# Optimization experiments

Hardware: AMD Instinct MI355X
Metric: run time of the kernel (lower is better)

Reference implementation:

```python
import jax, jax.numpy as jnp
import numpy as np

B, S, IN, D, H, L, M = 8, 1024, 256, 512, 8, 2, 64
DK = D // H
FF = 4 * D
EPS = 1e-5


def setup_inputs() -> dict:
    key = jax.random.key(0)
    ks = jax.random.split(key, 16)
    w = lambda k, shape: jax.random.normal(k, shape, jnp.float32) * 0.02
    return {
        "inputs": jax.random.normal(ks[0], (B, S, IN), jnp.float32),
        "lengths": jax.random.randint(ks[1], (B,), S // 2, S + 1),
        "W_in": w(ks[2], (IN, D)), "b_in": jnp.zeros((D,), jnp.float32),
        # per-layer stacked params (leading axis L) for lax.scan
        "Wq": w(ks[3], (L, D, D)), "bq": jnp.zeros((L, D), jnp.float32),
        "Wk": w(ks[4], (L, D, D)), "bk": jnp.zeros((L, D), jnp.float32),
        "Wv": w(ks[5], (L, D, D)), "bv": jnp.zeros((L, D), jnp.float32),
        "Wo": w(ks[6], (L, D, D)), "bo": jnp.zeros((L, D), jnp.float32),
        "rel_bias": w(ks[7], (L, H, 2 * M - 1)),
        "W1": w(ks[8], (L, D, FF)), "b1": jnp.zeros((L, FF), jnp.float32),
        "W2": w(ks[9], (L, FF, D)), "b2": jnp.zeros((L, D), jnp.float32),
        "g1": jnp.ones((L, D), jnp.float32), "be1": jnp.zeros((L, D), jnp.float32),
        "g2": jnp.ones((L, D), jnp.float32), "be2": jnp.zeros((L, D), jnp.float32),
        "gf": jnp.ones((D,), jnp.float32), "bef": jnp.zeros((D,), jnp.float32),
    }


def _ln(x, g, b):
    m = jnp.mean(x, axis=-1, keepdims=True)
    v = jnp.mean(jnp.square(x - m), axis=-1, keepdims=True)
    return (x - m) * jax.lax.rsqrt(v + EPS) * g + b


def _sinusoid_pe(seq_len, d_model):
    pos = jnp.arange(seq_len, dtype=jnp.float32)[:, None]
    div = jnp.exp(jnp.arange(0, d_model, 2, dtype=jnp.float32) * (-np.log(10000.0) / d_model))
    pe = jnp.zeros((seq_len, d_model), jnp.float32)
    pe = pe.at[:, 0::2].set(jnp.sin(pos * div))
    pe = pe.at[:, 1::2].set(jnp.cos(pos * div))
    return pe


def _encoder(inputs, lengths, W_in, b_in, Wq, bq, Wk, bk, Wv, bv, Wo, bo,
             rel_bias, W1, b1, W2, b2, g1, be1, g2, be2, gf, bef):
    x = inputs @ W_in + b_in                      # (B,S,D)
    x = x + _sinusoid_pe(S, D)[None]
    pad = jnp.arange(S)[None, :] >= lengths[:, None]   # (B,S) True = padded key

    r = jnp.arange(S)
    rel_idx = jnp.clip(r[:, None] - r[None, :], -(M - 1), M - 1) + (M - 1)  # (S,S)
    scale = 1.0 / np.sqrt(DK)

    def layer(x, p):
        (wq, bq_, wk, bk_, wv, bv_, wo, bo_, rb, w1, b1_, w2, b2_, g1_, be1_, g2_, be2_) = p
        # --- self-attention sublayer (pre-norm) ---
        h = _ln(x, g1_, be1_)
        q = (h @ wq + bq_).reshape(B, S, H, DK).transpose(0, 2, 1, 3)  # (B,H,S,DK)
        k = (h @ wk + bk_).reshape(B, S, H, DK).transpose(0, 2, 1, 3)
        v = (h @ wv + bv_).reshape(B, S, H, DK).transpose(0, 2, 1, 3)
        scores = jnp.einsum('bhqd,bhkd->bhqk', q, k) * scale
        scores = scores + rb[:, rel_idx][None]            # (H,S,S) relative bias
        scores = jnp.where(pad[:, None, None, :], -jnp.inf, scores)
        attn = jax.nn.softmax(scores, axis=-1)
        o = jnp.einsum('bhqk,bhkd->bhqd', attn, v)
        o = o.transpose(0, 2, 1, 3).reshape(B, S, D) @ wo + bo_
        x = x + o
        # --- FFN sublayer (pre-norm) ---
        h = _ln(x, g2_, be2_)
        x = x + (jax.nn.relu(h @ w1 + b1_) @ w2 + b2_)
        return x, None

    stacked = (Wq, bq, Wk, bk, Wv, bv, Wo, bo, rel_bias, W1, b1, W2, b2, g1, be1, g2, be2)
    x, _ = jax.lax.scan(layer, x, stacked)
    return _ln(x, gf, bef)


def reference(inputs, lengths, W_in, b_in, Wq, bq, Wk, bk, Wv, bv, Wo, bo,
              rel_bias, W1, b1, W2, b2, g1, be1, g2, be2, gf, bef):
    return _encoder(inputs, lengths, W_in, b_in, Wq, bq, Wk, bk, Wv, bv, Wo, bo,
                    rel_bias, W1, b1, W2, b2, g1, be1, g2, be2, gf, bef)
```

## Files before the change

kernel.cpp:

```cpp
#include <hip/hip_runtime.h>
#include <hip/hip_bf16.h>

typedef unsigned short u16;
typedef unsigned int u32;
typedef __bf16 v8bf __attribute__((ext_vector_type(8)));
typedef float v4f __attribute__((ext_vector_type(4)));

#define B_SZ 8
#define S_LEN 1024
#define IN_DIM 256
#define DMODEL 512
#define NHEAD 8
#define DK 64
#define FF_DIM 2048
#define MROWS (B_SZ * S_LEN)
#define QSCALE 0.1803368801111204f

__device__ __forceinline__ u16 f2bf(float f) {
    unsigned int x = __float_as_uint(f);
    unsigned int r = (x + 0x7fffu + ((x >> 16) & 1u)) >> 16;
    return (u16)r;
}

__device__ __forceinline__ void gl16(const u16* g, u16* l) {
    __builtin_amdgcn_global_load_lds((const __attribute__((address_space(1))) unsigned int*)g,
                                     (__attribute__((address_space(3))) unsigned int*)l, 16, 0, 0);
}

__global__ __launch_bounds__(256) void conv_bf16_kernel(const float* __restrict__ in,
                                                        u16* __restrict__ out, int n4) {
    int i = blockIdx.x * 256 + threadIdx.x;
    if (i < n4) {
        float4 v = ((const float4*)in)[i];
        ushort4 o;
        o.x = f2bf(v.x); o.y = f2bf(v.y); o.z = f2bf(v.z); o.w = f2bf(v.w);
        ((ushort4*)out)[i] = o;
    }
}

struct TDesc { const float* src; u16* dst; int K; int N; };
struct TArgs { TDesc d[13]; };

__global__ void transpose_conv_kernel(TArgs args) {
    TDesc t = args.d[blockIdx.z];
    int k0 = blockIdx.x * 32, n0 = blockIdx.y * 32;
    if (k0 >= t.K || n0 >= t.N) return;
    __shared__ float tile[32][33];
    int tx = threadIdx.x, ty = threadIdx.y;
#pragma unroll
    for (int j = 0; j < 4; j++) {
        int k = k0 + ty + j * 8;
        tile[ty + j * 8][tx] = t.src[(size_t)k * t.N + n0 + tx];
    }
    __syncthreads();
#pragma unroll
    for (int j = 0; j < 4; j++) {
        int n = n0 + ty + j * 8;
        t.dst[(size_t)n * t.K + k0 + tx] = f2bf(tile[tx][ty + j * 8]);
    }
}

template <bool OUT_BF16>
__global__ __launch_bounds__(256) void ln_kernel(const float* __restrict__ x,
                                                 const float* __restrict__ g,
                                                 const float* __restrict__ b,
                                                 void* __restrict__ out) {
    int row = blockIdx.x * 4 + (threadIdx.x >> 6);
    int lane = threadIdx.x & 63;
    const float4* xr = (const float4*)(x + (size_t)row * DMODEL);
    float4 v0 = xr[lane], v1 = xr[lane + 64];
    float s = v0.x + v0.y + v0.z + v0.w + v1.x + v1.y + v1.z + v1.w;
    float sq = v0.x * v0.x + v0.y * v0.y + v0.z * v0.z + v0.w * v0.w +
               v1.x * v1.x + v1.y * v1.y + v1.z * v1.z + v1.w * v1.w;
#pragma unroll
    for (int m = 1; m < 64; m <<= 1) {
        s += __shfl_xor(s, m);
        sq += __shfl_xor(sq, m);
    }
    float mean = s * (1.0f / DMODEL);
    float var = sq * (1.0f / DMODEL) - mean * mean;
    float rstd = rsqrtf(var + 1e-5f);
    const float4* g4 = (const float4*)g;
    const float4* b4 = (const float4*)b;
    float4 ga = g4[lane], gb = g4[lane + 64], ba = b4[lane], bb = b4[lane + 64];
    float4 r0, r1;
    r0.x = (v0.x - mean) * rstd * ga.x + ba.x;
    r0.y = (v0.y - mean) * rstd * ga.y + ba.y;
    r0.z = (v0.z - mean) * rstd * ga.z + ba.z;
    r0.w = (v0.w - mean) * rstd * ga.w + ba.w;
    r1.x = (v1.x - mean) * rstd * gb.x + bb.x;
    r1.y = (v1.y - mean) * rstd * gb.y + bb.y;
    r1.z = (v1.z - mean) * rstd * gb.z + bb.z;
    r1.w = (v1.w - mean) * rstd * gb.w + bb.w;
    if (OUT_BF16) {
        ushort4 o0, o1;
        o0.x = f2bf(r0.x); o0.y = f2bf(r0.y); o0.z = f2bf(r0.z); o0.w = f2bf(r0.w);
        o1.x = f2bf(r1.x); o1.y = f2bf(r1.y); o1.z = f2bf(r1.z); o1.w = f2bf(r1.w);
        ((ushort4*)out)[(size_t)row * 128 + lane] = o0;
        ((ushort4*)out)[(size_t)row * 128 + 64 + lane] = o1;
    } else {
        ((float4*)out)[(size_t)row * 128 + lane] = r0;
        ((float4*)out)[(size_t)row * 128 + 64 + lane] = r1;
    }
}

template <int MT, int NT>
__device__ __forceinline__ void gemm_core(const u16* __restrict__ A, const u16* __restrict__ Bt,
                                          int K, v4f (&acc)[MT][NT]) {
    constexpr int BM = MT * 32;
    constexpr int BN = NT * 32;
    __shared__ u16 As[BM * 64];
    __shared__ u16 Bs[BN * 64];
    int tid = threadIdx.x;
    int n0 = blockIdx.x * BN, m0 = blockIdx.y * BM;
    int w = tid >> 6, lane = tid & 63;
    int wr = (w >> 1) * (BM / 2), wc = (w & 1) * (BN / 2);
    int lr = lane & 15, lq = lane >> 4;
    int r8 = lane >> 3, cb = lane & 7;
    int scol = (cb ^ r8) * 8;

    v4f zero = {0.f, 0.f, 0.f, 0.f};
#pragma unroll
    for (int i = 0; i < MT; i++)
#pragma unroll
        for (int j = 0; j < NT; j++) acc[i][j] = zero;

    const u16* gA[MT]; u16* lA[MT];
#pragma unroll
    for (int j = 0; j < MT; j++) {
        int row0 = (MT * 8) * w + j * 8;
        gA[j] = A + (size_t)(m0 + row0 + r8) * K + scol;
        lA[j] = As + row0 * 64;
    }
    const u16* gB[NT]; u16* lB[NT];
#pragma unroll
    for (int j = 0; j < NT; j++) {
        int row0 = (NT * 8) * w + j * 8;
        gB[j] = Bt + (size_t)(n0 + row0 + r8) * K + scol;
        lB[j] = Bs + row0 * 64;
    }

    for (int k0 = 0; k0 < K; k0 += 64) {
#pragma unroll
        for (int j = 0; j < MT; j++) gl16(gA[j], lA[j]);
#pragma unroll
        for (int j = 0; j < NT; j++) gl16(gB[j], lB[j]);
        __syncthreads();
#pragma unroll
        for (int kk = 0; kk < 2; kk++) {
            int xb = ((kk * 4 + lq) ^ (lr & 7)) * 8;
            v8bf af[MT], bfr[NT];
#pragma unroll
            for (int i = 0; i < MT; i++)
                af[i] = *(const v8bf*)&As[(wr + i * 16 + lr) * 64 + xb];
#pragma unroll
            for (int j = 0; j < NT; j++)
                bfr[j] = *(const v8bf*)&Bs[(wc + j * 16 + lr) * 64 + xb];
#pragma unroll
            for (int mt = 0; mt < MT; mt++)
#pragma unroll
                for (int nt = 0; nt < NT; nt++)
                    acc[mt][nt] = __builtin_amdgcn_mfma_f32_16x16x32_bf16(af[mt], bfr[nt], acc[mt][nt], 0, 0, 0);
        }
        __syncthreads();
#pragma unroll
        for (int j = 0; j < MT; j++) gA[j] += 64;
#pragma unroll
        for (int j = 0; j < NT; j++) gB[j] += 64;
    }
}

__global__ __launch_bounds__(256) void gemm_in_kernel(const u16* __restrict__ A,
                                                      const u16* __restrict__ Bt,
                                                      const float* __restrict__ bias,
                                                      float* __restrict__ Out, int K) {
    v4f acc[4][2];
    gemm_core<4, 2>(A, Bt, K, acc);
    int tid = threadIdx.x, w = tid >> 6, lane = tid & 63;
    int lr = lane & 15, lq = lane >> 4;
    int wr = (w >> 1) * 64, wc = (w & 1) * 32;
    int n0 = blockIdx.x * 64, m0 = blockIdx.y * 128;
#pragma unroll
    for (int mt = 0; mt < 4; mt++) {
#pragma unroll
        for (int nt = 0; nt < 2; nt++) {
            int col = n0 + wc + nt * 16 + lr;
            float bcol = bias[col];
            float freq = __builtin_amdgcn_exp2f((float)(col & ~1) * (-0.025953277f));
#pragma unroll
            for (int reg = 0; reg < 4; reg++) {
                int row = m0 + wr + mt * 16 + lq * 4 + reg;
                float rev = (float)(row & (S_LEN - 1)) * freq * 0.15915494309189535f;
                float fr = __builtin_amdgcn_fractf(rev);
                float pe = (col & 1) ? __builtin_amdgcn_cosf(fr) : __builtin_amdgcn_sinf(fr);
                Out[(size_t)row * DMODEL + col] = acc[mt][nt][reg] + bcol + pe;
            }
        }
    }
}

__global__ __launch_bounds__(256) void gemm_qkv_kernel(const u16* __restrict__ A,
                                                       const u16* __restrict__ Bt,
                                                       const float* __restrict__ bq,
                                                       const float* __restrict__ bk,
                                                       const float* __restrict__ bv,
                                                       u16* __restrict__ Qo,
                                                       u16* __restrict__ Ko,
                                                       u16* __restrict__ Vto, int K) {
    v4f acc[4][4];
    gemm_core<4, 4>(A, Bt, K, acc);
    int tid = threadIdx.x, w = tid >> 6, lane = tid & 63;
    int lr = lane & 15, lq = lane >> 4;
    int wr = (w >> 1) * 64, wc = (w & 1) * 64;
    int n0 = blockIdx.x * 128, m0 = blockIdx.y * 128;
    int seg = n0 >> 9;
#pragma unroll
    for (int mt = 0; mt < 4; mt++) {
#pragma unroll
        for (int nt = 0; nt < 4; nt++) {
            int col = (n0 + wc + nt * 16 + lr) & (DMODEL - 1);
            if (seg == 0) {
                float bcol = bq[col];
#pragma unroll
                for (int reg = 0; reg < 4; reg++) {
                    int row = m0 + wr + mt * 16 + lq * 4 + reg;
                    Qo[(size_t)row * DMODEL + col] = f2bf((acc[mt][nt][reg] + bcol) * QSCALE);
                }
            } else if (seg == 1) {
                float bcol = bk[col];
#pragma unroll
                for (int reg = 0; reg < 4; reg++) {
                    int row = m0 + wr + mt * 16 + lq * 4 + reg;
                    Ko[(size_t)row * DMODEL + col] = f2bf(acc[mt][nt][reg] + bcol);
                }
            } else {
                float bcol = bv[col];
                int row0 = m0 + wr + mt * 16 + lq * 4;
                int bb = row0 >> 10, s0 = row0 & (S_LEN - 1);
                ushort4 o;
                o.x = f2bf(acc[mt][nt][0] + bcol);
                o.y = f2bf(acc[mt][nt][1] + bcol);
                o.z = f2bf(acc[mt][nt][2] + bcol);
                o.w = f2bf(acc[mt][nt][3] + bcol);
                *(ushort4*)(Vto + ((size_t)(bb * DMODEL + col)) * S_LEN + s0) = o;
            }
        }
    }
}

__global__ __launch_bounds__(256) void gemm_relu_kernel(const u16* __restrict__ A,
                                                        const u16* __restrict__ Bt,
                                                        const float* __restrict__ bias,
                                                        u16* __restrict__ Out, int N, int K) {
    v4f acc[4][4];
    gemm_core<4, 4>(A, Bt, K, acc);
    int tid = threadIdx.x, w = tid >> 6, lane = tid & 63;
    int lr = lane & 15, lq = lane >> 4;
    int wr = (w >> 1) * 64, wc = (w & 1) * 64;
    int n0 = blockIdx.x * 128, m0 = blockIdx.y * 128;
#pragma unroll
    for (int mt = 0; mt < 4; mt++) {
#pragma unroll
        for (int nt = 0; nt < 4; nt++) {
            int col = n0 + wc + nt * 16 + lr;
            float bcol = bias[col];
#pragma unroll
            for (int reg = 0; reg < 4; reg++) {
                int row = m0 + wr + mt * 16 + lq * 4 + reg;
                Out[(size_t)row * N + col] = f2bf(fmaxf(acc[mt][nt][reg] + bcol, 0.0f));
            }
        }
    }
}

__global__ __launch_bounds__(256) void gemm_res_kernel(const u16* __restrict__ A,
                                                       const u16* __restrict__ Bt,
                                                       const float* __restrict__ bias,
                                                       float* __restrict__ Out, int K) {
    v4f acc[4][2];
    gemm_core<4, 2>(A, Bt, K, acc);
    int tid = threadIdx.x, w = tid >> 6, lane = tid & 63;
    int lr = lane & 15, lq = lane >> 4;
    int wr = (w >> 1) * 64, wc = (w & 1) * 32;
    int n0 = blockIdx.x * 64, m0 = blockIdx.y * 128;
#pragma unroll
    for (int mt = 0; mt < 4; mt++) {
#pragma unroll
        for (int nt = 0; nt < 2; nt++) {
            int col = n0 + wc + nt * 16 + lr;
            float bcol = bias[col];
#pragma unroll
            for (int reg = 0; reg < 4; reg++) {
                int row = m0 + wr + mt * 16 + lq * 4 + reg;
                size_t idx = (size_t)row * DMODEL + col;
                Out[idx] = Out[idx] + acc[mt][nt][reg] + bcol;
            }
        }
    }
}

#define LDP 68
__global__ __launch_bounds__(256) void fattn_kernel(const u16* __restrict__ Qg,
                                                    const u16* __restrict__ Kg,
                                                    const u16* __restrict__ Vtg,
                                                    const float* __restrict__ rb,
                                                    const int* __restrict__ lengths,
                                                    u16* __restrict__ Op,
                                                    float* __restrict__ lsums) {
    int bid = blockIdx.x;
    int wg = (bid & 7) * 128 + (bid >> 3);
    int half = wg & 1;
    int qt = (wg >> 1) & 7;
    int bh = wg >> 4;
    int h = bh & 7, b = bh >> 3;
    int tid = threadIdx.x, w = tid >> 6, lane = tid & 63;
    int lr = lane & 15, lq = lane >> 4;
    __shared__ u16 Ks[2][64 * 64];
    __shared__ u16 Vs[2][64 * 64];
    __shared__ u16 Pw[4][32 * LDP];
    __shared__ float rbs[128];
    int len = lengths[b];
    if (tid < 127) rbs[tid] = rb[h * 127 + tid] * 1.4426950408889634f;

    int kstart = half * 512;
    int kend = half ? len : 512;

    int qw = qt * 128 + w * 32;
    v8bf qa[2][2];
#pragma unroll
    for (int ntq = 0; ntq < 2; ntq++) {
        size_t qrow = ((size_t)(b * S_LEN + qw + ntq * 16 + lr)) * DMODEL + h * DK;
        qa[ntq][0] = *(const v8bf*)(Qg + qrow + lq * 8);
        qa[ntq][1] = *(const v8bf*)(Qg + qrow + 32 + lq * 8);
    }

    v4f zero = {0.f, 0.f, 0.f, 0.f};
    v4f Oacc[2][4];
#pragma unroll
    for (int mt = 0; mt < 2; mt++)
#pragma unroll
        for (int nt = 0; nt < 4; nt++) Oacc[mt][nt] = zero;
    float lsum[2] = {0.f, 0.f};

    const u16* Kbase = Kg + ((size_t)b * S_LEN) * DMODEL + h * DK;
    const u16* Vbase = Vtg + ((size_t)(b * DMODEL + h * DK)) * S_LEN;
    u16* P = Pw[w];
    int r8 = lane >> 3, cb = lane & 7;
    int swz = (cb ^ r8) * 8;

#pragma unroll
    for (int j = 0; j < 2; j++) {
        int row0 = w * 16 + j * 8;
        gl16(Kbase + (size_t)(kstart + row0 + r8) * DMODEL + swz, Ks[0] + row0 * 64);
        gl16(Vbase + (size_t)(row0 + r8) * S_LEN + kstart + swz, Vs[0] + row0 * 64);
    }

    int pb = 0;
    for (int kb0 = kstart; kb0 < kend; kb0 += 64, pb ^= 1) {
        __syncthreads();
        __builtin_amdgcn_sched_barrier(0);

        int nxt = kb0 + 64;
        if (nxt < kend) {
#pragma unroll
            for (int j = 0; j < 2; j++) {
                int row0 = w * 16 + j * 8;
                gl16(Kbase + (size_t)(nxt + row0 + r8) * DMODEL + swz, Ks[pb ^ 1] + row0 * 64);
                gl16(Vbase + (size_t)(row0 + r8) * S_LEN + nxt + swz, Vs[pb ^ 1] + row0 * 64);
            }
        }
        const u16* Ksc = Ks[pb];
        const u16* Vsc = Vs[pb];

        v8bf kf[4][2];
#pragma unroll
        for (int mtk = 0; mtk < 4; mtk++) {
#pragma unroll
            for (int half_ = 0; half_ < 2; half_++) {
                int xb = ((half_ * 4 + lq) ^ (lr & 7)) * 8;
                kf[mtk][half_] = *(const v8bf*)&Ksc[(mtk * 16 + lr) * 64 + xb];
            }
        }

        v4f S[4][2];
        __builtin_amdgcn_s_setprio(1);
#pragma unroll
        for (int mtk = 0; mtk < 4; mtk++)
#pragma unroll
            for (int ntq = 0; ntq < 2; ntq++) {
                v4f s = __builtin_amdgcn_mfma_f32_16x16x32_bf16(kf[mtk][0], qa[ntq][0], zero, 0, 0, 0);
                S[mtk][ntq] = __builtin_amdgcn_mfma_f32_16x16x32_bf16(kf[mtk][1], qa[ntq][1], s, 0, 0, 0);
            }
        __builtin_amdgcn_s_setprio(0);

        bool edge = (kb0 + 64 > len);
        int dmin = qw - (kb0 + 63), dmax = qw + 31 - kb0;
        bool perel = !(dmax <= -63 || dmin >= 63);
        float bconst = (dmax <= -63) ? rbs[0] : rbs[126];
#pragma unroll
        for (int mtk = 0; mtk < 4; mtk++) {
#pragma unroll
            for (int ntq = 0; ntq < 2; ntq++) {
                int q = qw + ntq * 16 + lr;
                float p[4];
#pragma unroll
                for (int r = 0; r < 4; r++) {
                    int key = kb0 + mtk * 16 + lq * 4 + r;
                    float s = S[mtk][ntq][r];
                    if (perel) {
                        int d = q - key;
                        d = d < -63 ? -63 : (d > 63 ? 63 : d);
                        s += rbs[d + 63];
                    } else {
                        s += bconst;
                    }
                    float pv = __builtin_amdgcn_exp2f(s);
                    if (edge && key >= len) pv = 0.f;
                    lsum[ntq] += pv;
                    p[r] = pv;
                }
                uint2 pk;
                pk.x = (__float_as_uint(p[1]) & 0xffff0000u) | (__float_as_uint(p[0]) >> 16);
                pk.y = (__float_as_uint(p[3]) & 0xffff0000u) | (__float_as_uint(p[2]) >> 16);
                *(uint2*)&P[(ntq * 16 + lr) * LDP + mtk * 16 + lq * 4] = pk;
            }
        }

        v8bf vb[4][2];
#pragma unroll
        for (int ntd = 0; ntd < 4; ntd++) {
#pragma unroll
            for (int half_ = 0; half_ < 2; half_++) {
                int xb = ((half_ * 4 + lq) ^ (lr & 7)) * 8;
                vb[ntd][half_] = *(const v8bf*)&Vsc[(ntd * 16 + lr) * 64 + xb];
            }
        }
        __builtin_amdgcn_s_setprio(1);
#pragma unroll
        for (int mtq = 0; mtq < 2; mtq++) {
            v8bf pa0 = *(const v8bf*)&P[(mtq * 16 + lr) * LDP + lq * 8];
            v8bf pa1 = *(const v8bf*)&P[(mtq * 16 + lr) * LDP + 32 + lq * 8];
#pragma unroll
            for (int ntd = 0; ntd < 4; ntd++) {
                Oacc[mtq][ntd] = __builtin_amdgcn_mfma_f32_16x16x32_bf16(pa0, vb[ntd][0], Oacc[mtq][ntd], 0, 0, 0);
                Oacc[mtq][ntd] = __builtin_amdgcn_mfma_f32_16x16x32_bf16(pa1, vb[ntd][1], Oacc[mtq][ntd], 0, 0, 0);
            }
        }
        __builtin_amdgcn_s_setprio(0);
    }

    float lsumR[2];
#pragma unroll
    for (int ntq = 0; ntq < 2; ntq++) {
        float s = lsum[ntq];
        s += __shfl_xor(s, 16);
        s += __shfl_xor(s, 32);
        lsumR[ntq] = s;
    }
    if (lq == 0) {
#pragma unroll
        for (int ntq = 0; ntq < 2; ntq++) {
            int q = qw + ntq * 16 + lr;
            lsums[((size_t)half * MROWS + b * S_LEN + q) * NHEAD + h] = lsumR[ntq];
        }
    }
    u16* Oh = Op + (size_t)half * MROWS * DMODEL;
#pragma unroll
    for (int mtq = 0; mtq < 2; mtq++) {
        size_t obase = ((size_t)(b * S_LEN + qw + mtq * 16)) * DMODEL + h * DK;
#pragma unroll
        for (int ntd = 0; ntd < 4; ntd++)
#pragma unroll
            for (int r = 0; r < 4; r++)
                Oh[obase + (size_t)(lq * 4 + r) * DMODEL + ntd * 16 + lr] = f2bf(Oacc[mtq][ntd][r]);
    }
}

__device__ __forceinline__ u32 comb2(u32 a, u32 b, float inv) {
    float r0 = (__uint_as_float(a << 16) + __uint_as_float(b << 16)) * inv;
    float r1 = (__uint_as_float(a & 0xffff0000u) + __uint_as_float(b & 0xffff0000u)) * inv;
    return (u32)f2bf(r0) | ((u32)f2bf(r1) << 16);
}

__global__ __launch_bounds__(256) void attn_combine_kernel(const u16* __restrict__ Op,
                                                           const float* __restrict__ lsums,
                                                           u16* __restrict__ out) {
    int row = blockIdx.x * 4 + (threadIdx.x >> 6);
    int lane = threadIdx.x & 63;
    int h = lane >> 3;
    float l0 = lsums[(size_t)row * NHEAD + h];
    float l1 = lsums[((size_t)MROWS + row) * NHEAD + h];
    float inv = 1.0f / (l0 + l1);
    size_t base = (size_t)row * DMODEL + lane * 8;
    uint4 a = *(const uint4*)(Op + base);
    uint4 c = *(const uint4*)(Op + (size_t)MROWS * DMODEL + base);
    uint4 o;
    o.x = comb2(a.x, c.x, inv);
    o.y = comb2(a.y, c.y, inv);
    o.z = comb2(a.z, c.z, inv);
    o.w = comb2(a.w, c.w, inv);
    *(uint4*)(out + base) = o;
}

extern "C" void kernel_launch(void* const* d_in, const int* in_sizes, int n_in,
                              void* d_out, int out_size, void* d_ws, size_t ws_size,
                              hipStream_t stream) {
    const float* inputs   = (const float*)d_in[0];
    const int*   lengths  = (const int*)d_in[1];
    const float* W_in     = (const float*)d_in[2];
    const float* b_in     = (const float*)d_in[3];
    const float* Wq       = (const float*)d_in[4];
    const float* bq       = (const float*)d_in[5];
    const float* Wk       = (const float*)d_in[6];
    const float* bk       = (const float*)d_in[7];
    const float* Wv       = (const float*)d_in[8];
    const float* bv       = (const float*)d_in[9];
    const float* Wo       = (const float*)d_in[10];
    const float* bo       = (const float*)d_in[11];
    const float* rel_bias = (const float*)d_in[12];
    const float* W1       = (const float*)d_in[13];
    const float* b1       = (const float*)d_in[14];
    const float* W2       = (const float*)d_in[15];
    const float* b2       = (const float*)d_in[16];
    const float* g1       = (const float*)d_in[17];
    const float* be1      = (const float*)d_in[18];
    const float* g2       = (const float*)d_in[19];
    const float* be2      = (const float*)d_in[20];
    const float* gf       = (const float*)d_in[21];
    const float* bef      = (const float*)d_in[22];

    char* ws = (char*)d_ws;
    float* xbuf = (float*)ws;          ws += (size_t)MROWS * DMODEL * 4;
    u16* hbuf   = (u16*)ws;            ws += (size_t)MROWS * DMODEL * 2;
    u16* aobuf  = hbuf;
    u16* qbf    = (u16*)ws;            ws += (size_t)MROWS * FF_DIM * 2;
    u16* kbf    = qbf + (size_t)MROWS * DMODEL;
    u16* vtbf   = kbf + (size_t)MROWS * DMODEL;
    float* lsums = (float*)(vtbf + (size_t)MROWS * DMODEL);
    u16* tbuf   = qbf;
    u16* inbf   = qbf;
    u16* opart  = (u16*)d_out;
    u16* wt_in  = (u16*)ws;            ws += (size_t)DMODEL * IN_DIM * 2;
    u16 *qkvw[2], *wto[2], *wt1[2], *wt2[2];
    for (int l = 0; l < 2; l++) { qkvw[l] = (u16*)ws; ws += (size_t)3 * DMODEL * DMODEL * 2; }
    for (int l = 0; l < 2; l++) { wto[l] = (u16*)ws; ws += (size_t)DMODEL * DMODEL * 2; }
    for (int l = 0; l < 2; l++) { wt1[l] = (u16*)ws; ws += (size_t)FF_DIM * DMODEL * 2; }
    for (int l = 0; l < 2; l++) { wt2[l] = (u16*)ws; ws += (size_t)DMODEL * FF_DIM * 2; }

    TArgs ta;
    int ti = 0;
    ta.d[ti++] = {W_in, wt_in, IN_DIM, DMODEL};
    for (int l = 0; l < 2; l++) {
        ta.d[ti++] = {Wq + (size_t)l * DMODEL * DMODEL, qkvw[l], DMODEL, DMODEL};
        ta.d[ti++] = {Wk + (size_t)l * DMODEL * DMODEL, qkvw[l] + (size_t)DMODEL * DMODEL, DMODEL, DMODEL};
        ta.d[ti++] = {Wv + (size_t)l * DMODEL * DMODEL, qkvw[l] + (size_t)2 * DMODEL * DMODEL, DMODEL, DMODEL};
        ta.d[ti++] = {Wo + (size_t)l * DMODEL * DMODEL, wto[l], DMODEL, DMODEL};
        ta.d[ti++] = {W1 + (size_t)l * DMODEL * FF_DIM, wt1[l], DMODEL, FF_DIM};
        ta.d[ti++] = {W2 + (size_t)l * FF_DIM * DMODEL, wt2[l], FF_DIM, DMODEL};
    }

    conv_bf16_kernel<<<dim3((MROWS * IN_DIM / 4 + 255) / 256), 256, 0, stream>>>(
        inputs, inbf, MROWS * IN_DIM / 4);
    transpose_conv_kernel<<<dim3(64, 64, 13), dim3(32, 8), 0, stream>>>(ta);

    gemm_in_kernel<<<dim3(DMODEL / 64, MROWS / 128), 256, 0, stream>>>(
        inbf, wt_in, b_in, xbuf, IN_DIM);

    for (int l = 0; l < 2; l++) {
        ln_kernel<true><<<MROWS / 4, 256, 0, stream>>>(xbuf, g1 + l * DMODEL, be1 + l * DMODEL, hbuf);
        gemm_qkv_kernel<<<dim3(3 * DMODEL / 128, MROWS / 128), 256, 0, stream>>>(
            hbuf, qkvw[l], bq + l * DMODEL, bk + l * DMODEL, bv + l * DMODEL,
            qbf, kbf, vtbf, DMODEL);
        fattn_kernel<<<dim3(1024), 256, 0, stream>>>(
            qbf, kbf, vtbf, rel_bias + (size_t)l * NHEAD * 127, lengths, opart, lsums);
        attn_combine_kernel<<<MROWS / 4, 256, 0, stream>>>(opart, lsums, aobuf);
        gemm_res_kernel<<<dim3(DMODEL / 64, MROWS / 128), 256, 0, stream>>>(
            aobuf, wto[l], bo + l * DMODEL, xbuf, DMODEL);
        ln_kernel<true><<<MROWS / 4, 256, 0, stream>>>(xbuf, g2 + l * DMODEL, be2 + l * DMODEL, hbuf);
        gemm_relu_kernel<<<dim3(FF_DIM / 128, MROWS / 128), 256, 0, stream>>>(
            hbuf, wt1[l], b1 + l * FF_DIM, tbuf, FF_DIM, DMODEL);
        gemm_res_kernel<<<dim3(DMODEL / 64, MROWS / 128), 256, 0, stream>>>(
            tbuf, wt2[l], b2 + l * DMODEL, xbuf, FF_DIM);
    }
    ln_kernel<false><<<MROWS / 4, 256, 0, stream>>>(xbuf, gf, bef, d_out);
}
```

Measured before the change: 495.7 us.

## Keep attention probabilities in registers and balance key split by sequence length

The flash-attention kernel no longer stages P through shared memory. The exp'd scores stay in registers and feed the PV MFMA directly, with V read from LDS as the A operand and the output accumulator transposed to match. The key range is now split at half the padded length instead of a fixed 512, so both halves do similar work. The block-to-work mapping changes, launch bounds request 4 waves per SIMD, and output stores become 8-byte vector writes. The transposed V fragment gather uses narrower 8-byte LDS reads, and the occupancy hint may force register spills.

```diff
diff --git a/kernel.cpp b/kernel.cpp
--- a/kernel.cpp
+++ b/kernel.cpp
@@ -299,31 +299,31 @@
     }
 }
 
-#define LDP 68
-__global__ __launch_bounds__(256) void fattn_kernel(const u16* __restrict__ Qg,
-                                                    const u16* __restrict__ Kg,
-                                                    const u16* __restrict__ Vtg,
-                                                    const float* __restrict__ rb,
-                                                    const int* __restrict__ lengths,
-                                                    u16* __restrict__ Op,
-                                                    float* __restrict__ lsums) {
+__global__ __launch_bounds__(256, 4) void fattn_kernel(const u16* __restrict__ Qg,
+                                                       const u16* __restrict__ Kg,
+                                                       const u16* __restrict__ Vtg,
+                                                       const float* __restrict__ rb,
+                                                       const int* __restrict__ lengths,
+                                                       u16* __restrict__ Op,
+                                                       float* __restrict__ lsums) {
     int bid = blockIdx.x;
     int wg = (bid & 7) * 128 + (bid >> 3);
-    int half = wg & 1;
-    int qt = (wg >> 1) & 7;
-    int bh = wg >> 4;
-    int h = bh & 7, b = bh >> 3;
+    int i = wg & 127;
+    int h = wg >> 7;
+    int b = i & 7;
+    int qt = (i >> 3) & 7;
+    int kvh = (i >> 6) & 1;
     int tid = threadIdx.x, w = tid >> 6, lane = tid & 63;
     int lr = lane & 15, lq = lane >> 4;
     __shared__ u16 Ks[2][64 * 64];
     __shared__ u16 Vs[2][64 * 64];
-    __shared__ u16 Pw[4][32 * LDP];
     __shared__ float rbs[128];
     int len = lengths[b];
     if (tid < 127) rbs[tid] = rb[h * 127 + tid] * 1.4426950408889634f;
 
-    int kstart = half * 512;
-    int kend = half ? len : 512;
+    int l2 = ((len + 127) >> 7) << 6;
+    int kstart = kvh ? l2 : 0;
+    int kend = kvh ? len : l2;
 
     int qw = qt * 128 + w * 32;
     v8bf qa[2][2];
@@ -335,16 +335,15 @@
     }
 
     v4f zero = {0.f, 0.f, 0.f, 0.f};
-    v4f Oacc[2][4];
-#pragma unroll
-    for (int mt = 0; mt < 2; mt++)
-#pragma unroll
-        for (int nt = 0; nt < 4; nt++) Oacc[mt][nt] = zero;
+    v4f Oacc[4][2];
+#pragma unroll
+    for (int dt = 0; dt < 4; dt++)
+#pragma unroll
+        for (int nt = 0; nt < 2; nt++) Oacc[dt][nt] = zero;
     float lsum[2] = {0.f, 0.f};
 
     const u16* Kbase = Kg + ((size_t)b * S_LEN) * DMODEL + h * DK;
     const u16* Vbase = Vtg + ((size_t)(b * DMODEL + h * DK)) * S_LEN;
-    u16* P = Pw[w];
     int r8 = lane >> 3, cb = lane & 7;
     int swz = (cb ^ r8) * 8;
 
@@ -372,31 +371,27 @@
         const u16* Ksc = Ks[pb];
         const u16* Vsc = Vs[pb];
 
-        v8bf kf[4][2];
-#pragma unroll
-        for (int mtk = 0; mtk < 4; mtk++) {
-#pragma unroll
-            for (int half_ = 0; half_ < 2; half_++) {
-                int xb = ((half_ * 4 + lq) ^ (lr & 7)) * 8;
-                kf[mtk][half_] = *(const v8bf*)&Ksc[(mtk * 16 + lr) * 64 + xb];
-            }
-        }
-
         v4f S[4][2];
         __builtin_amdgcn_s_setprio(1);
 #pragma unroll
-        for (int mtk = 0; mtk < 4; mtk++)
+        for (int mtk = 0; mtk < 4; mtk++) {
+            int xb0 = (lq ^ (lr & 7)) * 8;
+            int xb1 = ((4 + lq) ^ (lr & 7)) * 8;
+            v8bf kf0 = *(const v8bf*)&Ksc[(mtk * 16 + lr) * 64 + xb0];
+            v8bf kf1 = *(const v8bf*)&Ksc[(mtk * 16 + lr) * 64 + xb1];
 #pragma unroll
             for (int ntq = 0; ntq < 2; ntq++) {
-                v4f s = __builtin_amdgcn_mfma_f32_16x16x32_bf16(kf[mtk][0], qa[ntq][0], zero, 0, 0, 0);
-                S[mtk][ntq] = __builtin_amdgcn_mfma_f32_16x16x32_bf16(kf[mtk][1], qa[ntq][1], s, 0, 0, 0);
-            }
+                v4f s = __builtin_amdgcn_mfma_f32_16x16x32_bf16(kf0, qa[ntq][0], zero, 0, 0, 0);
+                S[mtk][ntq] = __builtin_amdgcn_mfma_f32_16x16x32_bf16(kf1, qa[ntq][1], s, 0, 0, 0);
+            }
+        }
         __builtin_amdgcn_s_setprio(0);
 
         bool edge = (kb0 + 64 > len);
         int dmin = qw - (kb0 + 63), dmax = qw + 31 - kb0;
         bool perel = !(dmax <= -63 || dmin >= 63);
         float bconst = (dmax <= -63) ? rbs[0] : rbs[126];
+        uint2 pks[4][2];
 #pragma unroll
         for (int mtk = 0; mtk < 4; mtk++) {
 #pragma unroll
@@ -419,31 +414,29 @@
                     lsum[ntq] += pv;
                     p[r] = pv;
                 }
-                uint2 pk;
-                pk.x = (__float_as_uint(p[1]) & 0xffff0000u) | (__float_as_uint(p[0]) >> 16);
-                pk.y = (__float_as_uint(p[3]) & 0xffff0000u) | (__float_as_uint(p[2]) >> 16);
-                *(uint2*)&P[(ntq * 16 + lr) * LDP + mtk * 16 + lq * 4] = pk;
-            }
-        }
-
-        v8bf vb[4][2];
-#pragma unroll
-        for (int ntd = 0; ntd < 4; ntd++) {
-#pragma unroll
-            for (int half_ = 0; half_ < 2; half_++) {
-                int xb = ((half_ * 4 + lq) ^ (lr & 7)) * 8;
-                vb[ntd][half_] = *(const v8bf*)&Vsc[(ntd * 16 + lr) * 64 + xb];
-            }
-        }
+                pks[mtk][ntq].x = (__float_as_uint(p[1]) & 0xffff0000u) | (__float_as_uint(p[0]) >> 16);
+                pks[mtk][ntq].y = (__float_as_uint(p[3]) & 0xffff0000u) | (__float_as_uint(p[2]) >> 16);
+            }
+        }
+
         __builtin_amdgcn_s_setprio(1);
 #pragma unroll
-        for (int mtq = 0; mtq < 2; mtq++) {
-            v8bf pa0 = *(const v8bf*)&P[(mtq * 16 + lr) * LDP + lq * 8];
-            v8bf pa1 = *(const v8bf*)&P[(mtq * 16 + lr) * LDP + 32 + lq * 8];
-#pragma unroll
-            for (int ntd = 0; ntd < 4; ntd++) {
-                Oacc[mtq][ntd] = __builtin_amdgcn_mfma_f32_16x16x32_bf16(pa0, vb[ntd][0], Oacc[mtq][ntd], 0, 0, 0);
-                Oacc[mtq][ntd] = __builtin_amdgcn_mfma_f32_16x16x32_bf16(pa1, vb[ntd][1], Oacc[mtq][ntd], 0, 0, 0);
+        for (int kh = 0; kh < 2; kh++) {
+            uint4 tp0 = {pks[kh * 2][0].x, pks[kh * 2][0].y, pks[kh * 2 + 1][0].x, pks[kh * 2 + 1][0].y};
+            uint4 tp1 = {pks[kh * 2][1].x, pks[kh * 2][1].y, pks[kh * 2 + 1][1].x, pks[kh * 2 + 1][1].y};
+            v8bf pb0 = *(v8bf*)&tp0;
+            v8bf pb1 = *(v8bf*)&tp1;
+            int gl = kh * 4 + (lq >> 1);
+            int sub = (lq & 1) * 4;
+#pragma unroll
+            for (int dt = 0; dt < 4; dt++) {
+                int drow = (dt * 16 + lr) * 64;
+                uint2 lo = *(const uint2*)&Vsc[drow + ((gl ^ (lr & 7)) * 8 + sub)];
+                uint2 hi = *(const uint2*)&Vsc[drow + (((gl + 2) ^ (lr & 7)) * 8 + sub)];
+                uint4 tv = {lo.x, lo.y, hi.x, hi.y};
+                v8bf va = *(v8bf*)&tv;
+                Oacc[dt][0] = __builtin_amdgcn_mfma_f32_16x16x32_bf16(va, pb0, Oacc[dt][0], 0, 0, 0);
+                Oacc[dt][1] = __builtin_amdgcn_mfma_f32_16x16x32_bf16(va, pb1, Oacc[dt][1], 0, 0, 0);
             }
         }
         __builtin_amdgcn_s_setprio(0);
@@ -461,18 +454,22 @@
 #pragma unroll
         for (int ntq = 0; ntq < 2; ntq++) {
             int q = qw + ntq * 16 + lr;
-            lsums[((size_t)half * MROWS + b * S_LEN + q) * NHEAD + h] = lsumR[ntq];
-        }
-    }
-    u16* Oh = Op + (size_t)half * MROWS * DMODEL;
-#pragma unroll
-    for (int mtq = 0; mtq < 2; mtq++) {
-        size_t obase = ((size_t)(b * S_LEN + qw + mtq * 16)) * DMODEL + h * DK;
-#pragma unroll
-        for (int ntd = 0; ntd < 4; ntd++)
-#pragma unroll
-            for (int r = 0; r < 4; r++)
-                Oh[obase + (size_t)(lq * 4 + r) * DMODEL + ntd * 16 + lr] = f2bf(Oacc[mtq][ntd][r]);
+            lsums[((size_t)kvh * MROWS + b * S_LEN + q) * NHEAD + h] = lsumR[ntq];
+        }
+    }
+    u16* Oh = Op + (size_t)kvh * MROWS * DMODEL;
+#pragma unroll
+    for (int dt = 0; dt < 4; dt++) {
+#pragma unroll
+        for (int ntq = 0; ntq < 2; ntq++) {
+            size_t off = (size_t)(b * S_LEN + qw + ntq * 16 + lr) * DMODEL + h * DK + dt * 16 + lq * 4;
+            ushort4 o;
+            o.x = f2bf(Oacc[dt][ntq][0]);
+            o.y = f2bf(Oacc[dt][ntq][1]);
+            o.z = f2bf(Oacc[dt][ntq][2]);
+            o.w = f2bf(Oacc[dt][ntq][3]);
+            *(ushort4*)(Oh + off) = o;
+        }
     }
 }
 
```

Result: faster. 467.2 us (-5.7%).
